# Performance work log

Measured on AMD Instinct MI355X. Metric: run time of the kernel, lower is better.

The kernel has to match this reference:

```python
import jax, jax.numpy as jnp
import numpy as np

BS, S, L, D, P = 8, 32, 128, 768, 496  # batch, sent_len_max, seq_len, hidden, max pairs


def setup_inputs() -> dict:
    key = jax.random.key(0)
    ks = jax.random.split(key, 6)
    x_single = jax.random.normal(ks[0], (BS, S, L, D), dtype=jnp.float32)
    x_cls = jax.random.normal(ks[1], (BS, P, 1, D), dtype=jnp.float32)
    # attention mask: 1 = keep, 0 = masked
    sentence_attn_mask = (jax.random.uniform(ks[2], (BS, S, L)) > 0.1).astype(jnp.float32)
    W1 = jax.random.normal(ks[3], (D, D), dtype=jnp.float32) / np.sqrt(D)
    b1 = jnp.zeros((D,), dtype=jnp.float32)
    w2 = jax.random.normal(ks[4], (D,), dtype=jnp.float32) / np.sqrt(D)
    b2 = jnp.zeros((), dtype=jnp.float32)
    # unique (i, j) pairs per batch row so the torch overwrite-scatter equals an add-scatter
    rng = np.random.default_rng(0)
    flat = np.stack([rng.permutation(S * S)[:P] for _ in range(BS)])  # [BS, P]
    pairs_list = jnp.asarray(np.stack([flat // S, flat % S], axis=-1), dtype=jnp.int32)  # [BS, P, 2]
    pairs_num = jnp.asarray(rng.integers(P // 2, P + 1, size=BS), dtype=jnp.int32)
    return dict(x_single=x_single, x_cls=x_cls, sentence_attn_mask=sentence_attn_mask,
                W1=W1, b1=b1, w2=w2, b2=b2, pairs_list=pairs_list, pairs_num=pairs_num)


def reference(x_single, x_cls, sentence_attn_mask, W1, b1, w2, b2, pairs_list, pairs_num):
    # tanh-MLP attention scoring over tokens of each sentence
    h = jnp.tanh(jnp.einsum('bsld,dh->bslh', x_single, W1) + b1)       # [B,S,L,D]
    scores = jnp.einsum('bslh,h->bsl', h, w2) + b2                      # [B,S,L]
    scores = scores + (1.0 - sentence_attn_mask) * (-10000.0)
    probs = jax.nn.softmax(scores, axis=-1)                             # dropout in eval mode = identity
    final_sent = jnp.einsum('bsl,bslh->bsh', probs, x_single)           # [B,S,D]

    # ragged scatter of per-pair CLS vectors into [B,S,S,D]
    cls_pooled = x_cls[:, :, 0, :]                                      # [B,P,D]
    valid = jnp.arange(P)[None, :] < pairs_num[:, None]                 # [B,P]
    vals = jnp.where(valid[:, :, None], cls_pooled, 0.0)
    b_idx = jnp.broadcast_to(jnp.arange(BS)[:, None], (BS, P))
    cls_output_matrix_nn = jnp.zeros((BS, S, S, D), dtype=x_cls.dtype).at[
        b_idx, pairs_list[..., 0], pairs_list[..., 1]].add(vals)
    return final_sent, cls_output_matrix_nn
```

## Files before the change

kernel.cpp:

```cpp
#include <hip/hip_runtime.h>
#include <hip/hip_bf16.h>
#include <stdint.h>

#define BS 8
#define S  32
#define L  128
#define D  768
#define P  496

typedef float  f32x4  __attribute__((ext_vector_type(4)));
typedef __bf16 bf16x8 __attribute__((ext_vector_type(8)));
typedef __bf16 bf16x4 __attribute__((ext_vector_type(4)));

__global__ void k_zero(float4* __restrict__ p, int n) {
  int i = blockIdx.x * blockDim.x + threadIdx.x;
  if (i < n) p[i] = make_float4(0.f, 0.f, 0.f, 0.f);
}

__global__ void k_w1t(const float* __restrict__ w1, __bf16* __restrict__ w1t) {
  int idx = blockIdx.x * 256 + threadIdx.x;
  int h = idx / D, d = idx - h * D;
  w1t[idx] = (__bf16)w1[d * D + h];
}

__global__ void k_cvt(const float4* __restrict__ x, bf16x4* __restrict__ xb, int n4) {
  for (int i = blockIdx.x * blockDim.x + threadIdx.x; i < n4; i += gridDim.x * blockDim.x) {
    float4 v = x[i];
    bf16x4 h = { (__bf16)v.x, (__bf16)v.y, (__bf16)v.z, (__bf16)v.w };
    xb[i] = h;
  }
}

__global__ void k_scatter(const float4* __restrict__ xcls, const int* __restrict__ pairs,
                          const int* __restrict__ pnum, float4* __restrict__ outc) {
  int p = blockIdx.x, b = blockIdx.y;
  if (p >= pnum[b]) return;
  int i = pairs[(b * P + p) * 2 + 0];
  int j = pairs[(b * P + p) * 2 + 1];
  const float4* src = xcls + (size_t)(b * P + p) * (D / 4);
  float4*       dst = outc + (size_t)((b * S + i) * S + j) * (D / 4);
  dst[threadIdx.x] = src[threadIdx.x];
}

#define GEMM_LDS 65536

__global__ __launch_bounds__(256) void k_gemm_scores(
    const __bf16* __restrict__ xb, const __bf16* __restrict__ w1t,
    const float* __restrict__ b1, const float* __restrict__ w2,
    float* __restrict__ scores)
{
  extern __shared__ char smem[];

  int bid = blockIdx.x;
  int swz = (bid & 7) * 192 + (bid >> 3);
  int bm = swz / 6, bn = swz - 6 * bm;

  const int tid  = threadIdx.x;
  const int lane = tid & 63, wv = tid >> 6;
  const int wm = wv >> 1, wn = wv & 1;
  const int lo = lane & 15, kg = lane >> 4;

  const char* Ag[4];
  const char* Bg[4];
  #pragma unroll
  for (int inst = 0; inst < 4; ++inst) {
    int o  = inst * 4096 + tid * 16;
    int r  = o >> 7;
    int c2 = (o >> 4) & 7;
    int sc = c2 ^ (r & 7);
    Ag[inst] = (const char*)xb  + (size_t)(bm * 128 + r) * (D * 2) + sc * 16;
    Bg[inst] = (const char*)w1t + (size_t)(bn * 128 + r) * (D * 2) + sc * 16;
  }

  auto STAGE = [&](int buf, int t) {
    char* la = smem + buf * 32768 + wv * 1024;
    char* lb = la + 16384;
    const size_t koff = (size_t)t * 128;
    #pragma unroll
    for (int inst = 0; inst < 4; ++inst) {
      __builtin_amdgcn_global_load_lds(
          (const __attribute__((address_space(1))) void*)(Ag[inst] + koff),
          (__attribute__((address_space(3))) void*)(la + inst * 4096), 16, 0, 0);
      __builtin_amdgcn_global_load_lds(
          (const __attribute__((address_space(1))) void*)(Bg[inst] + koff),
          (__attribute__((address_space(3))) void*)(lb + inst * 4096), 16, 0, 0);
    }
  };

  f32x4 acc[4][4];
  #pragma unroll
  for (int mf = 0; mf < 4; ++mf)
    #pragma unroll
    for (int nf = 0; nf < 4; ++nf)
      acc[mf][nf] = (f32x4){0.f, 0.f, 0.f, 0.f};

  STAGE(0, 0);
  __syncthreads();

  for (int t = 0; t < 12; ++t) {
    const int cur = t & 1;
    if (t < 11) STAGE(cur ^ 1, t + 1);

    const char* As = smem + cur * 32768;
    const char* Bs = As + 16384;
    bf16x8 a[4][2], b[4][2];
    #pragma unroll
    for (int mf = 0; mf < 4; ++mf)
      #pragma unroll
      for (int kk = 0; kk < 2; ++kk)
        a[mf][kk] = *(const bf16x8*)(As + (wm * 64 + mf * 16 + lo) * 128
                                        + (((kk * 4 + kg) ^ (lo & 7)) * 16));
    #pragma unroll
    for (int nf = 0; nf < 4; ++nf)
      #pragma unroll
      for (int kk = 0; kk < 2; ++kk)
        b[nf][kk] = *(const bf16x8*)(Bs + (wn * 64 + nf * 16 + lo) * 128
                                        + (((kk * 4 + kg) ^ (lo & 7)) * 16));
    #pragma unroll
    for (int kk = 0; kk < 2; ++kk)
      #pragma unroll
      for (int mf = 0; mf < 4; ++mf)
        #pragma unroll
        for (int nf = 0; nf < 4; ++nf)
          acc[mf][nf] = __builtin_amdgcn_mfma_f32_16x16x32_bf16(a[mf][kk], b[nf][kk], acc[mf][nf], 0, 0, 0);

    __syncthreads();
  }

  float part[4][4];
  #pragma unroll
  for (int mf = 0; mf < 4; ++mf)
    #pragma unroll
    for (int r = 0; r < 4; ++r) part[mf][r] = 0.f;

  #pragma unroll
  for (int nf = 0; nf < 4; ++nf) {
    int n = bn * 128 + wn * 64 + nf * 16 + lo;
    float b1v = b1[n], w2v = w2[n];
    #pragma unroll
    for (int mf = 0; mf < 4; ++mf)
      #pragma unroll
      for (int r = 0; r < 4; ++r) {
        float z = acc[mf][nf][r] + b1v;
        float e = __expf(2.f * z);
        part[mf][r] += w2v * (1.f - 2.f / (e + 1.f));
      }
  }
  #pragma unroll
  for (int mf = 0; mf < 4; ++mf)
    #pragma unroll
    for (int r = 0; r < 4; ++r) {
      float v = part[mf][r];
      v += __shfl_xor(v, 1);
      v += __shfl_xor(v, 2);
      v += __shfl_xor(v, 4);
      v += __shfl_xor(v, 8);
      part[mf][r] = v;
    }
  if (lo == 0) {
    int rowb = bm * 128 + wm * 64;
    #pragma unroll
    for (int mf = 0; mf < 4; ++mf)
      #pragma unroll
      for (int r = 0; r < 4; ++r)
        atomicAdd(&scores[rowb + mf * 16 + kg * 4 + r], part[mf][r]);
  }
}

__global__ void k_probs(const float* __restrict__ scores, const float* __restrict__ mask,
                        float* __restrict__ probs) {
  int bs = blockIdx.x, t = threadIdx.x;
  __shared__ float sc[L];
  float s = scores[bs * L + t] + (1.f - mask[bs * L + t]) * -10000.f;
  sc[t] = s;
  __syncthreads();
  float mx = -1e30f;
  #pragma unroll 8
  for (int l = 0; l < L; ++l) mx = fmaxf(mx, sc[l]);
  float sum = 0.f;
  #pragma unroll 8
  for (int l = 0; l < L; ++l) sum += __expf(sc[l] - mx);
  probs[bs * L + t] = __expf(s - mx) / sum;
}

__global__ void k_final(const __bf16* __restrict__ xb, const float* __restrict__ probs,
                        float* __restrict__ out) {
  int bs = blockIdx.x;
  int t  = threadIdx.x;
  __shared__ float p[L];
  if (t < L) p[t] = probs[bs * L + t];
  __syncthreads();
  const bf16x4* xp = (const bf16x4*)(xb + (size_t)bs * L * D) + t;
  float4 acc = make_float4(0.f, 0.f, 0.f, 0.f);
  #pragma unroll 4
  for (int l = 0; l < L; ++l) {
    bf16x4 v = xp[(size_t)l * (D / 4)];
    float pl = p[l];
    acc.x += pl * (float)v[0];
    acc.y += pl * (float)v[1];
    acc.z += pl * (float)v[2];
    acc.w += pl * (float)v[3];
  }
  ((float4*)(out + (size_t)bs * D))[t] = acc;
}

extern "C" void kernel_launch(void* const* d_in, const int* in_sizes, int n_in,
                              void* d_out, int out_size, void* d_ws, size_t ws_size,
                              hipStream_t stream) {
  const float* x    = (const float*)d_in[0];
  const float* xcls = (const float*)d_in[1];
  const float* mask = (const float*)d_in[2];
  const float* w1   = (const float*)d_in[3];
  const float* b1   = (const float*)d_in[4];
  const float* w2   = (const float*)d_in[5];
  const int* pairs  = (const int*)d_in[7];
  const int* pnum   = (const int*)d_in[8];

  float* out_final = (float*)d_out;
  float* out_cls   = (float*)d_out + (size_t)BS * S * D;

  __bf16* xb    = (__bf16*)d_ws;
  __bf16* w1t   = (__bf16*)((char*)d_ws + (size_t)BS * S * L * D * 2);
  float* scores = (float*)((char*)w1t + (size_t)D * D * 2);
  float* probs  = scores + BS * S * L;

  {
    int n = (BS * S * S * D) / 4;
    k_zero<<<(n + 255) / 256, 256, 0, stream>>>((float4*)out_cls, n);
  }
  {
    int n = (BS * S * L) / 4;
    k_zero<<<(n + 255) / 256, 256, 0, stream>>>((float4*)scores, n);
  }
  k_w1t<<<(D * D) / 256, 256, 0, stream>>>(w1, w1t);
  k_cvt<<<2048, 256, 0, stream>>>((const float4*)x, (bf16x4*)xb, (BS * S * L * D) / 4);
  k_scatter<<<dim3(P, BS), D / 4, 0, stream>>>((const float4*)xcls, pairs, pnum, (float4*)out_cls);

  hipFuncSetAttribute((const void*)k_gemm_scores, hipFuncAttributeMaxDynamicSharedMemorySize, GEMM_LDS);
  k_gemm_scores<<<(32768 / 128) * (D / 128), 256, GEMM_LDS, stream>>>(xb, w1t, b1, w2, scores);

  k_probs<<<BS * S, L, 0, stream>>>(scores, mask, probs);
  k_final<<<BS * S, 192, 0, stream>>>(xb, probs, out_final);
}
```

Baseline: 270.6 us.

## Fuse prep kernels, halve GEMM K-tile for occupancy, merge softmax with pooling

Merges W1 transpose, scores zeroing and the x-to-bf16 conversion into one launch, and fuses the softmax and probability-weighted pooling kernels into one. The GEMM K-tile drops from 128 to 64 (24 iterations, 32 KB LDS, no XOR swizzle) with launch bounds requesting 5 blocks per SM for higher occupancy. The pooling kernel now uses 384 threads reading two bf16 values each. The goal is to cut launch overhead and intermediate traffic and to hide latency better, at the cost of more barriers per GEMM and possible LDS bank conflicts from the unswizzled 64-byte rows.

```diff
diff --git a/kernel.cpp b/kernel.cpp
--- a/kernel.cpp
+++ b/kernel.cpp
@@ -17,14 +17,21 @@
   if (i < n) p[i] = make_float4(0.f, 0.f, 0.f, 0.f);
 }
 
-__global__ void k_w1t(const float* __restrict__ w1, __bf16* __restrict__ w1t) {
-  int idx = blockIdx.x * 256 + threadIdx.x;
-  int h = idx / D, d = idx - h * D;
-  w1t[idx] = (__bf16)w1[d * D + h];
-}
-
-__global__ void k_cvt(const float4* __restrict__ x, bf16x4* __restrict__ xb, int n4) {
-  for (int i = blockIdx.x * blockDim.x + threadIdx.x; i < n4; i += gridDim.x * blockDim.x) {
+#define PREP_CVT_BASE 2336
+#define PREP_NBLK (PREP_CVT_BASE + 24576)
+__global__ void k_prep(const float* __restrict__ w1, __bf16* __restrict__ w1t,
+                       float4* __restrict__ scores4,
+                       const float4* __restrict__ x, bf16x4* __restrict__ xb) {
+  int blk = blockIdx.x, tid = threadIdx.x;
+  if (blk < 2304) {
+    int idx = blk * 256 + tid;
+    int h = idx / D, d = idx - h * D;
+    w1t[idx] = (__bf16)w1[d * D + h];
+  } else if (blk < PREP_CVT_BASE) {
+    int i = (blk - 2304) * 256 + tid;
+    if (i < (BS * S * L) / 4) scores4[i] = make_float4(0.f, 0.f, 0.f, 0.f);
+  } else {
+    int i = (blk - PREP_CVT_BASE) * 256 + tid;
     float4 v = x[i];
     bf16x4 h = { (__bf16)v.x, (__bf16)v.y, (__bf16)v.z, (__bf16)v.w };
     xb[i] = h;
@@ -42,9 +49,9 @@
   dst[threadIdx.x] = src[threadIdx.x];
 }
 
-#define GEMM_LDS 65536
-
-__global__ __launch_bounds__(256) void k_gemm_scores(
+#define GEMM_LDS 32768
+
+__global__ __launch_bounds__(256, 5) void k_gemm_scores(
     const __bf16* __restrict__ xb, const __bf16* __restrict__ w1t,
     const float* __restrict__ b1, const float* __restrict__ w2,
     float* __restrict__ scores)
@@ -60,30 +67,30 @@
   const int wm = wv >> 1, wn = wv & 1;
   const int lo = lane & 15, kg = lane >> 4;
 
-  const char* Ag[4];
-  const char* Bg[4];
-  #pragma unroll
-  for (int inst = 0; inst < 4; ++inst) {
-    int o  = inst * 4096 + tid * 16;
-    int r  = o >> 7;
-    int c2 = (o >> 4) & 7;
-    int sc = c2 ^ (r & 7);
-    Ag[inst] = (const char*)xb  + (size_t)(bm * 128 + r) * (D * 2) + sc * 16;
-    Bg[inst] = (const char*)w1t + (size_t)(bn * 128 + r) * (D * 2) + sc * 16;
+  const char* Ag[2];
+  const char* Bg[2];
+  int ldsOff[2];
+  #pragma unroll
+  for (int inst = 0; inst < 2; ++inst) {
+    int o = inst * 4096 + tid * 16;
+    int r = o >> 6;
+    int c = (o >> 4) & 3;
+    Ag[inst] = (const char*)xb  + (size_t)(bm * 128 + r) * (D * 2) + c * 16;
+    Bg[inst] = (const char*)w1t + (size_t)(bn * 128 + r) * (D * 2) + c * 16;
+    ldsOff[inst] = inst * 4096 + wv * 1024;
   }
 
   auto STAGE = [&](int buf, int t) {
-    char* la = smem + buf * 32768 + wv * 1024;
-    char* lb = la + 16384;
-    const size_t koff = (size_t)t * 128;
-    #pragma unroll
-    for (int inst = 0; inst < 4; ++inst) {
+    char* base = smem + buf * 16384;
+    const size_t koff = (size_t)t * 64;
+    #pragma unroll
+    for (int inst = 0; inst < 2; ++inst) {
       __builtin_amdgcn_global_load_lds(
           (const __attribute__((address_space(1))) void*)(Ag[inst] + koff),
-          (__attribute__((address_space(3))) void*)(la + inst * 4096), 16, 0, 0);
+          (__attribute__((address_space(3))) void*)(base + ldsOff[inst]), 16, 0, 0);
       __builtin_amdgcn_global_load_lds(
           (const __attribute__((address_space(1))) void*)(Bg[inst] + koff),
-          (__attribute__((address_space(3))) void*)(lb + inst * 4096), 16, 0, 0);
+          (__attribute__((address_space(3))) void*)(base + 8192 + ldsOff[inst]), 16, 0, 0);
     }
   };
 
@@ -97,32 +104,24 @@
   STAGE(0, 0);
   __syncthreads();
 
-  for (int t = 0; t < 12; ++t) {
+  for (int t = 0; t < 24; ++t) {
     const int cur = t & 1;
-    if (t < 11) STAGE(cur ^ 1, t + 1);
-
-    const char* As = smem + cur * 32768;
-    const char* Bs = As + 16384;
-    bf16x8 a[4][2], b[4][2];
+    if (t < 23) STAGE(cur ^ 1, t + 1);
+
+    const char* As = smem + cur * 16384;
+    const char* Bs = As + 8192;
+    bf16x8 a[4], b[4];
+    #pragma unroll
+    for (int mf = 0; mf < 4; ++mf)
+      a[mf] = *(const bf16x8*)(As + (wm * 64 + mf * 16 + lo) * 64 + kg * 16);
+    #pragma unroll
+    for (int nf = 0; nf < 4; ++nf)
+      b[nf] = *(const bf16x8*)(Bs + (wn * 64 + nf * 16 + lo) * 64 + kg * 16);
     #pragma unroll
     for (int mf = 0; mf < 4; ++mf)
       #pragma unroll
-      for (int kk = 0; kk < 2; ++kk)
-        a[mf][kk] = *(const bf16x8*)(As + (wm * 64 + mf * 16 + lo) * 128
-                                        + (((kk * 4 + kg) ^ (lo & 7)) * 16));
-    #pragma unroll
-    for (int nf = 0; nf < 4; ++nf)
-      #pragma unroll
-      for (int kk = 0; kk < 2; ++kk)
-        b[nf][kk] = *(const bf16x8*)(Bs + (wn * 64 + nf * 16 + lo) * 128
-                                        + (((kk * 4 + kg) ^ (lo & 7)) * 16));
-    #pragma unroll
-    for (int kk = 0; kk < 2; ++kk)
-      #pragma unroll
-      for (int mf = 0; mf < 4; ++mf)
-        #pragma unroll
-        for (int nf = 0; nf < 4; ++nf)
-          acc[mf][nf] = __builtin_amdgcn_mfma_f32_16x16x32_bf16(a[mf][kk], b[nf][kk], acc[mf][nf], 0, 0, 0);
+      for (int nf = 0; nf < 4; ++nf)
+        acc[mf][nf] = __builtin_amdgcn_mfma_f32_16x16x32_bf16(a[mf], b[nf], acc[mf][nf], 0, 0, 0);
 
     __syncthreads();
   }
@@ -167,41 +166,36 @@
   }
 }
 
-__global__ void k_probs(const float* __restrict__ scores, const float* __restrict__ mask,
-                        float* __restrict__ probs) {
+__global__ __launch_bounds__(384) void k_probs_final(
+    const float* __restrict__ scores, const float* __restrict__ mask,
+    const __bf16* __restrict__ xb, float* __restrict__ out)
+{
   int bs = blockIdx.x, t = threadIdx.x;
   __shared__ float sc[L];
-  float s = scores[bs * L + t] + (1.f - mask[bs * L + t]) * -10000.f;
-  sc[t] = s;
+  __shared__ float p[L];
+  if (t < L) sc[t] = scores[bs * L + t] + (1.f - mask[bs * L + t]) * -10000.f;
   __syncthreads();
-  float mx = -1e30f;
-  #pragma unroll 8
-  for (int l = 0; l < L; ++l) mx = fmaxf(mx, sc[l]);
-  float sum = 0.f;
-  #pragma unroll 8
-  for (int l = 0; l < L; ++l) sum += __expf(sc[l] - mx);
-  probs[bs * L + t] = __expf(s - mx) / sum;
-}
-
-__global__ void k_final(const __bf16* __restrict__ xb, const float* __restrict__ probs,
-                        float* __restrict__ out) {
-  int bs = blockIdx.x;
-  int t  = threadIdx.x;
-  __shared__ float p[L];
-  if (t < L) p[t] = probs[bs * L + t];
+  if (t < L) {
+    float mx = -1e30f;
+    #pragma unroll 8
+    for (int l = 0; l < L; ++l) mx = fmaxf(mx, sc[l]);
+    float sum = 0.f;
+    #pragma unroll 8
+    for (int l = 0; l < L; ++l) sum += __expf(sc[l] - mx);
+    p[t] = __expf(sc[t] - mx) / sum;
+  }
   __syncthreads();
-  const bf16x4* xp = (const bf16x4*)(xb + (size_t)bs * L * D) + t;
-  float4 acc = make_float4(0.f, 0.f, 0.f, 0.f);
+
+  const uint32_t* xp = (const uint32_t*)(xb + (size_t)bs * L * D) + t;
+  float a0 = 0.f, a1 = 0.f;
   #pragma unroll 4
   for (int l = 0; l < L; ++l) {
-    bf16x4 v = xp[(size_t)l * (D / 4)];
+    uint32_t u = xp[(size_t)l * (D / 2)];
     float pl = p[l];
-    acc.x += pl * (float)v[0];
-    acc.y += pl * (float)v[1];
-    acc.z += pl * (float)v[2];
-    acc.w += pl * (float)v[3];
-  }
-  ((float4*)(out + (size_t)bs * D))[t] = acc;
+    a0 += pl * __uint_as_float(u << 16);
+    a1 += pl * __uint_as_float(u & 0xffff0000u);
+  }
+  ((float2*)(out + (size_t)bs * D))[t] = make_float2(a0, a1);
 }
 
 extern "C" void kernel_launch(void* const* d_in, const int* in_sizes, int n_in,
@@ -222,23 +216,15 @@
   __bf16* xb    = (__bf16*)d_ws;
   __bf16* w1t   = (__bf16*)((char*)d_ws + (size_t)BS * S * L * D * 2);
   float* scores = (float*)((char*)w1t + (size_t)D * D * 2);
-  float* probs  = scores + BS * S * L;
 
   {
     int n = (BS * S * S * D) / 4;
     k_zero<<<(n + 255) / 256, 256, 0, stream>>>((float4*)out_cls, n);
   }
-  {
-    int n = (BS * S * L) / 4;
-    k_zero<<<(n + 255) / 256, 256, 0, stream>>>((float4*)scores, n);
-  }
-  k_w1t<<<(D * D) / 256, 256, 0, stream>>>(w1, w1t);
-  k_cvt<<<2048, 256, 0, stream>>>((const float4*)x, (bf16x4*)xb, (BS * S * L * D) / 4);
+  k_prep<<<PREP_NBLK, 256, 0, stream>>>(w1, w1t, (float4*)scores, (const float4*)x, (bf16x4*)xb);
   k_scatter<<<dim3(P, BS), D / 4, 0, stream>>>((const float4*)xcls, pairs, pnum, (float4*)out_cls);
 
-  hipFuncSetAttribute((const void*)k_gemm_scores, hipFuncAttributeMaxDynamicSharedMemorySize, GEMM_LDS);
   k_gemm_scores<<<(32768 / 128) * (D / 128), 256, GEMM_LDS, stream>>>(xb, w1t, b1, w2, scores);
 
-  k_probs<<<BS * S, L, 0, stream>>>(scores, mask, probs);
-  k_final<<<BS * S, 192, 0, stream>>>(xb, probs, out_final);
-}
+  k_probs_final<<<BS * S, 384, 0, stream>>>(scores, mask, xb, out_final);
+}
```

After: 303.6 us. 1.12x slower.
